# Performance work log

Measured on AMD Instinct MI355X. Metric: run time of the kernel, lower is better.

Reference implementation:

```python
import jax, jax.numpy as jnp
import numpy as np

TAU = 1.0
EPS = 1e-8  # F.cosine_similarity eps


def _cl(X, Y):
    # Pairwise cosine similarity via L2-normalize + single GEMM (N,D)@(D,N)
    Xn = X / jnp.maximum(jnp.linalg.norm(X, axis=1, keepdims=True), EPS)
    Yn = Y / jnp.maximum(jnp.linalg.norm(Y, axis=1, keepdims=True), EPS)
    sim = Xn @ Yn.T  # [N, N], sim[i, j] = cos(X_i, Y_j)
    e = jnp.exp(sim / TAU)
    pos = jnp.diagonal(e)               # exp(diag(sim)/tau), [N]
    neg = jnp.sum(e, axis=0) - pos      # column sums minus positive, [N]
    return -jnp.log(pos / neg).reshape(X.shape[0], 1)


def setup_inputs() -> dict:
    key = jax.random.key(0)
    ks = jax.random.split(key, 6)
    N, D1, D2, DO = 8192, 1024, 768, 256
    X = jax.random.normal(ks[0], (N, D1), dtype=jnp.float32)
    Y = jax.random.normal(ks[1], (N, D2), dtype=jnp.float32)
    # nn.Linear params (kaiming-uniform-ish scale)
    Wx = jax.random.uniform(ks[2], (DO, D1), jnp.float32, -1, 1) / np.sqrt(D1)
    bx = jax.random.uniform(ks[3], (DO,), jnp.float32, -1, 1) / np.sqrt(D1)
    Wy = jax.random.uniform(ks[4], (DO, D2), jnp.float32, -1, 1) / np.sqrt(D2)
    by = jax.random.uniform(ks[5], (DO,), jnp.float32, -1, 1) / np.sqrt(D2)
    return {"X": X, "Y": Y, "Wx": Wx, "bx": bx, "Wy": Wy, "by": by}


def reference(X, Y, Wx, bx, Wy, by):
    Xp = X @ Wx.T + bx  # proj_x
    Yp = Y @ Wy.T + by  # proj_y
    return _cl(Xp, Yp) + _cl(Yp, Xp)  # [N, 1]
```

## Files before the change

### kernel.cpp

```cpp
#include <hip/hip_runtime.h>
#include <hip/hip_bf16.h>

typedef __bf16 bf16_t;
typedef __bf16 bf16x8 __attribute__((ext_vector_type(8)));
typedef float  f32x4  __attribute__((ext_vector_type(4)));
typedef unsigned long u64;
typedef u64 u64x2 __attribute__((ext_vector_type(2)));

__device__ __forceinline__ bf16x8 pack8(f32x4 a, f32x4 b) {
    bf16x8 h = { (bf16_t)a.x, (bf16_t)a.y, (bf16_t)a.z, (bf16_t)a.w,
                 (bf16_t)b.x, (bf16_t)b.y, (bf16_t)b.z, (bf16_t)b.w };
    return h;
}

__device__ __forceinline__ void gl_lds16(const void* g, void* l) {
    __builtin_amdgcn_global_load_lds(
        (const __attribute__((address_space(1))) unsigned int*)g,
        (__attribute__((address_space(3))) unsigned int*)l, 16, 0, 0);
}

#if __has_builtin(__builtin_amdgcn_cvt_pk_fp8_f32)
__device__ __forceinline__ unsigned char cvt1_e4m3(float x) {
    return (unsigned char)(__builtin_amdgcn_cvt_pk_fp8_f32(x, x, 0, false) & 0xff);
}
#else
__device__ __forceinline__ unsigned char cvt1_e4m3(float x) {
    unsigned u = __float_as_uint(x);
    unsigned sign = (u >> 24) & 0x80u;
    float a = fabsf(x);
    if (a < 7.8125e-3f) { int q = (int)(a * 512.0f + 0.5f); return (unsigned char)(sign | q); }
    if (a >= 448.0f) return (unsigned char)(sign | 0x7E);
    unsigned au = u & 0x7FFFFFFFu;
    unsigned lsb = (au >> 20) & 1u;
    au += 0x7FFFFu + lsb;
    int exp = (int)(au >> 23) - 127;
    unsigned man = (au >> 20) & 7u;
    return (unsigned char)(sign | ((unsigned)(exp + 7) << 3) | man);
}
#endif

__device__ __forceinline__ int frag_off_k(int row16, int k) {
    return ((k >> 6) << 10) + (((k >> 3) & 3) << 8) + (row16 << 4)
         + (((k >> 5) & 1) << 3) + (k & 7);
}

__global__ __launch_bounds__(256) void wconv(
    const float* __restrict__ Wx, const float* __restrict__ Wy,
    bf16_t* __restrict__ Wxt, bf16_t* __restrict__ Wyt,
    float* __restrict__ sums)
{
    int id = blockIdx.x * 256 + threadIdx.x;
    if (blockIdx.x < 64) sums[id] = 0.0f;

    int row, k0, K;
    const float* W;
    bf16_t* Wt;
    if (id < 32768) { W = Wx; Wt = Wxt; K = 1024; row = id >> 7; k0 = (id & 127) << 3; }
    else { int c = id - 32768; W = Wy; Wt = Wyt; K = 768; row = c / 96; k0 = (c % 96) << 3; }

    f32x4 lo = *reinterpret_cast<const f32x4*>(&W[(size_t)row * K + k0]);
    f32x4 hi = *reinterpret_cast<const f32x4*>(&W[(size_t)row * K + k0 + 4]);
    size_t off = (size_t)(row >> 4) * 16 * K + frag_off_k(row & 15, k0);
    *reinterpret_cast<bf16x8*>(Wt + off) = pack8(lo, hi);
}

__global__ __launch_bounds__(512, 4) void proj_norm(
    const float* __restrict__ X, const float* __restrict__ Y,
    const bf16_t* __restrict__ Wxt, const float* __restrict__ bxp,
    const bf16_t* __restrict__ Wyt, const float* __restrict__ byp,
    unsigned char* __restrict__ Xt, unsigned char* __restrict__ Yt)
{
    __shared__ float Abuf[2][32 * 64];
    __shared__ unsigned char obuf[8192];
    __shared__ float ssqL[4][32];

    const int tid  = threadIdx.x;
    const int lane = tid & 63;
    const int wave = tid >> 6;
    const int quad = lane >> 4;
    const int c16  = lane & 15;
    const int rg   = wave >> 2;
    const int cg   = wave & 3;

    const bool isY = blockIdx.x >= 256;
    const float*  A    = isY ? Y   : X;
    const bf16_t* Wt   = isY ? Wyt : Wxt;
    const float*  bias = isY ? byp : bxp;
    unsigned char* dst = isY ? Yt  : Xt;
    const int K = isY ? 768 : 1024;
    const int S = K >> 6;
    const int rowBase = (blockIdx.x & 255) * 32;

    auto stage = [&](int s, int b) {
        int r0  = wave * 4;
        int row = r0 + (lane >> 4);
        int gch = (lane & 15) ^ (row & 15);
        gl_lds16(&A[(size_t)(rowBase + row) * K + s * 64 + gch * 4],
                 &Abuf[b][r0 * 64]);
    };

    auto aFrag = [&](int b, int s2) -> bf16x8 {
        int row = rg * 16 + c16;
        int e   = s2 * 8 + quad * 2;
        const float* base = &Abuf[b][row * 64];
        f32x4 lo = *reinterpret_cast<const f32x4*>(base + ((e ^ c16) << 2));
        f32x4 hi = *reinterpret_cast<const f32x4*>(base + (((e + 1) ^ c16) << 2));
        return pack8(lo, hi);
    };

    const bf16_t* pB[4];
    #pragma unroll
    for (int nf = 0; nf < 4; ++nf)
        pB[nf] = Wt + (size_t)(cg * 4 + nf) * 16 * K + quad * 256 + c16 * 16;

    f32x4 acc[4] = {};
    stage(0, 0);

    for (int s = 0; s < S; ++s) {
        const int b = s & 1;
        __syncthreads();
        if (s + 1 < S) stage(s + 1, b ^ 1);
        #pragma unroll
        for (int s2 = 0; s2 < 2; ++s2) {
            bf16x8 aF = aFrag(b, s2);
            #pragma unroll
            for (int nf = 0; nf < 4; ++nf) {
                bf16x8 bF = *reinterpret_cast<const bf16x8*>(pB[nf] + s * 1024 + s2 * 8);
                acc[nf] = __builtin_amdgcn_mfma_f32_16x16x32_bf16(aF, bF, acc[nf], 0, 0, 0);
            }
        }
    }

    #pragma unroll
    for (int nf = 0; nf < 4; ++nf) {
        float bb = bias[cg * 64 + nf * 16 + c16];
        #pragma unroll
        for (int r = 0; r < 4; ++r) acc[nf][r] += bb;
    }

    #pragma unroll
    for (int r = 0; r < 4; ++r) {
        float v = 0.f;
        #pragma unroll
        for (int nf = 0; nf < 4; ++nf) v += acc[nf][r] * acc[nf][r];
        v += __shfl_xor(v, 1, 64);
        v += __shfl_xor(v, 2, 64);
        v += __shfl_xor(v, 4, 64);
        v += __shfl_xor(v, 8, 64);
        if (c16 == 0) ssqL[cg][rg * 16 + quad * 4 + r] = v;
    }
    __syncthreads();

    #pragma unroll
    for (int r = 0; r < 4; ++r) {
        int lr = rg * 16 + quad * 4 + r;
        float t = ssqL[0][lr] + ssqL[1][lr] + ssqL[2][lr] + ssqL[3][lr];
        float inv = 1.0f / fmaxf(sqrtf(t), 1e-8f);
        #pragma unroll
        for (int nf = 0; nf < 4; ++nf) {
            int k = cg * 64 + nf * 16 + c16;
            obuf[((lr >> 4) << 12) + frag_off_k(lr & 15, k)] =
                cvt1_e4m3(acc[nf][r] * inv);
        }
    }
    __syncthreads();

    const f32x4* src = reinterpret_cast<const f32x4*>(&obuf[tid * 16]);
    f32x4* g = reinterpret_cast<f32x4*>(dst + (size_t)rowBase * 256 + tid * 16);
    g[0] = src[0];
}

__global__ __launch_bounds__(256) void sim_gemm(
    const unsigned char* __restrict__ Xt, const unsigned char* __restrict__ Yt,
    float* __restrict__ rowsum, float* __restrict__ colsum,
    float* __restrict__ pos)
{
    __shared__ float red[256];

    const int tid  = threadIdx.x;
    const int lane = tid & 63;
    const int wave = tid >> 6;
    const int quad = lane >> 4;
    const int c16  = lane & 15;
    const int wy   = wave >> 1;
    const int wx   = wave & 1;
    const int rowBase = blockIdx.x * 128;
    const int colBase = blockIdx.y * 128;

    const u64x2* pa[4];
    const u64x2* pb[4];
    #pragma unroll
    for (int mf = 0; mf < 4; ++mf)
        pa[mf] = reinterpret_cast<const u64x2*>(
            Xt + (size_t)(rowBase + wy * 64 + mf * 16) * 256 + quad * 256 + c16 * 16);
    #pragma unroll
    for (int nf = 0; nf < 4; ++nf)
        pb[nf] = reinterpret_cast<const u64x2*>(
            Yt + (size_t)(colBase + wx * 64 + nf * 16) * 256 + quad * 256 + c16 * 16);

    f32x4 acc[4][4] = {};

    auto loadf = [&](u64x2* A, u64x2* B, int slab) {
        #pragma unroll
        for (int i = 0; i < 4; ++i) {
            A[i] = pa[i][slab * 64];
            B[i] = pb[i][slab * 64];
        }
    };
    auto mm = [&](const u64x2* A, const u64x2* B) {
        #pragma unroll
        for (int mf = 0; mf < 4; ++mf)
            #pragma unroll
            for (int nf = 0; nf < 4; ++nf)
                acc[mf][nf] = __builtin_amdgcn_mfma_f32_16x16x32_fp8_fp8(
                    (long)A[mf].x, (long)B[nf].x, acc[mf][nf], 0, 0, 0);
        #pragma unroll
        for (int mf = 0; mf < 4; ++mf)
            #pragma unroll
            for (int nf = 0; nf < 4; ++nf)
                acc[mf][nf] = __builtin_amdgcn_mfma_f32_16x16x32_fp8_fp8(
                    (long)A[mf].y, (long)B[nf].y, acc[mf][nf], 0, 0, 0);
    };

    u64x2 A0[4], B0[4], A1[4], B1[4];
    loadf(A0, B0, 0);
    loadf(A1, B1, 1);
    mm(A0, B0);
    loadf(A0, B0, 2);
    mm(A1, B1);
    loadf(A1, B1, 3);
    mm(A0, B0);
    mm(A1, B1);

    #pragma unroll
    for (int mf = 0; mf < 4; ++mf)
        #pragma unroll
        for (int nf = 0; nf < 4; ++nf)
            #pragma unroll
            for (int r = 0; r < 4; ++r)
                acc[mf][nf][r] = __expf(acc[mf][nf][r]);

    if (rowBase == colBase) {
        #pragma unroll
        for (int mf = 0; mf < 4; ++mf)
            #pragma unroll
            for (int nf = 0; nf < 4; ++nf)
                #pragma unroll
                for (int r = 0; r < 4; ++r) {
                    int lrow = wy * 64 + mf * 16 + quad * 4 + r;
                    int lcol = wx * 64 + nf * 16 + c16;
                    if (lrow == lcol) pos[rowBase + lrow] = acc[mf][nf][r];
                }
    }

    float rs[4][4];
    #pragma unroll
    for (int mf = 0; mf < 4; ++mf)
        #pragma unroll
        for (int r = 0; r < 4; ++r) {
            float v = acc[mf][0][r] + acc[mf][1][r] + acc[mf][2][r] + acc[mf][3][r];
            v += __shfl_xor(v, 1, 64);
            v += __shfl_xor(v, 2, 64);
            v += __shfl_xor(v, 4, 64);
            v += __shfl_xor(v, 8, 64);
            rs[mf][r] = v;
        }

    float cs[4];
    #pragma unroll
    for (int nf = 0; nf < 4; ++nf) {
        float v = 0.f;
        #pragma unroll
        for (int mf = 0; mf < 4; ++mf)
            #pragma unroll
            for (int r = 0; r < 4; ++r)
                v += acc[mf][nf][r];
        v += __shfl_xor(v, 16, 64);
        v += __shfl_xor(v, 32, 64);
        cs[nf] = v;
    }

    red[tid] = 0.f;
    __syncthreads();

    if (c16 == 0) {
        #pragma unroll
        for (int mf = 0; mf < 4; ++mf)
            #pragma unroll
            for (int r = 0; r < 4; ++r)
                atomicAdd(&red[wy * 64 + mf * 16 + quad * 4 + r], rs[mf][r]);
    }
    if (quad == 0) {
        #pragma unroll
        for (int nf = 0; nf < 4; ++nf)
            atomicAdd(&red[128 + wx * 64 + nf * 16 + c16], cs[nf]);
    }
    __syncthreads();

    if (tid < 128) atomicAdd(&rowsum[rowBase + tid], red[tid]);
    else           atomicAdd(&colsum[colBase + tid - 128], red[tid]);
}

__global__ __launch_bounds__(256) void finalize(
    const float* __restrict__ rowsum, const float* __restrict__ colsum,
    const float* __restrict__ pos, float* __restrict__ out)
{
    int i = blockIdx.x * 256 + threadIdx.x;
    float p = pos[i];
    out[i] = logf(colsum[i] - p) + logf(rowsum[i] - p) - 2.0f * logf(p);
}

extern "C" void kernel_launch(void* const* d_in, const int* in_sizes, int n_in,
                              void* d_out, int out_size, void* d_ws, size_t ws_size,
                              hipStream_t stream) {
    const float* X  = (const float*)d_in[0];
    const float* Y  = (const float*)d_in[1];
    const float* Wx = (const float*)d_in[2];
    const float* bx = (const float*)d_in[3];
    const float* Wy = (const float*)d_in[4];
    const float* by = (const float*)d_in[5];
    float* out = (float*)d_out;

    char* ws = (char*)d_ws;
    unsigned char* Xt  = (unsigned char*)(ws);
    unsigned char* Yt  = (unsigned char*)(ws + (2u << 20));
    bf16_t*        Wxt = (bf16_t*)(ws + (4u << 20));
    bf16_t*        Wyt = (bf16_t*)(ws + (4u << 20) + (512u << 10));
    float* rowsum = (float*)(ws + (5u << 20));
    float* colsum = rowsum + 8192;
    float* pos    = colsum + 8192;

    wconv<<<224, 256, 0, stream>>>(Wx, Wy, Wxt, Wyt, rowsum);
    proj_norm<<<512, 512, 0, stream>>>(X, Y, Wxt, bx, Wyt, by, Xt, Yt);
    sim_gemm<<<dim3(64, 64), 256, 0, stream>>>(Xt, Yt, rowsum, colsum, pos);
    finalize<<<32, 256, 0, stream>>>(rowsum, colsum, pos, out);
}
```

Before: 172.1 us.

## Load projection A operands directly to registers with register double-buffering

The projection kernel drops the LDS staging of X/Y tiles via global_load_lds and __syncthreads, and instead has each lane load its A fragment straight from global memory into registers. A and B fragments are double-buffered in registers across K-steps. Blocks shrink to 256 threads covering 16 rows, with twice as many blocks launched. This removes per-step barriers and LDS traffic, but the fp32 A rows are now read with strided per-lane accesses and register pressure goes up.

```diff
diff --git a/kernel.cpp b/kernel.cpp
--- a/kernel.cpp
+++ b/kernel.cpp
@@ -11,12 +11,6 @@
     bf16x8 h = { (bf16_t)a.x, (bf16_t)a.y, (bf16_t)a.z, (bf16_t)a.w,
                  (bf16_t)b.x, (bf16_t)b.y, (bf16_t)b.z, (bf16_t)b.w };
     return h;
-}
-
-__device__ __forceinline__ void gl_lds16(const void* g, void* l) {
-    __builtin_amdgcn_global_load_lds(
-        (const __attribute__((address_space(1))) unsigned int*)g,
-        (__attribute__((address_space(3))) unsigned int*)l, 16, 0, 0);
 }
 
 #if __has_builtin(__builtin_amdgcn_cvt_pk_fp8_f32)
@@ -64,71 +58,73 @@
     *reinterpret_cast<bf16x8*>(Wt + off) = pack8(lo, hi);
 }
 
-__global__ __launch_bounds__(512, 4) void proj_norm(
+__global__ __launch_bounds__(256) void proj_norm(
     const float* __restrict__ X, const float* __restrict__ Y,
     const bf16_t* __restrict__ Wxt, const float* __restrict__ bxp,
     const bf16_t* __restrict__ Wyt, const float* __restrict__ byp,
     unsigned char* __restrict__ Xt, unsigned char* __restrict__ Yt)
 {
-    __shared__ float Abuf[2][32 * 64];
-    __shared__ unsigned char obuf[8192];
-    __shared__ float ssqL[4][32];
+    __shared__ unsigned char obuf[4096];
+    __shared__ float ssqL[4][16];
 
     const int tid  = threadIdx.x;
     const int lane = tid & 63;
-    const int wave = tid >> 6;
+    const int cg   = tid >> 6;
     const int quad = lane >> 4;
     const int c16  = lane & 15;
-    const int rg   = wave >> 2;
-    const int cg   = wave & 3;
-
-    const bool isY = blockIdx.x >= 256;
+
+    const bool isY = blockIdx.x >= 512;
     const float*  A    = isY ? Y   : X;
     const bf16_t* Wt   = isY ? Wyt : Wxt;
     const float*  bias = isY ? byp : bxp;
     unsigned char* dst = isY ? Yt  : Xt;
     const int K = isY ? 768 : 1024;
     const int S = K >> 6;
-    const int rowBase = (blockIdx.x & 255) * 32;
-
-    auto stage = [&](int s, int b) {
-        int r0  = wave * 4;
-        int row = r0 + (lane >> 4);
-        int gch = (lane & 15) ^ (row & 15);
-        gl_lds16(&A[(size_t)(rowBase + row) * K + s * 64 + gch * 4],
-                 &Abuf[b][r0 * 64]);
-    };
-
-    auto aFrag = [&](int b, int s2) -> bf16x8 {
-        int row = rg * 16 + c16;
-        int e   = s2 * 8 + quad * 2;
-        const float* base = &Abuf[b][row * 64];
-        f32x4 lo = *reinterpret_cast<const f32x4*>(base + ((e ^ c16) << 2));
-        f32x4 hi = *reinterpret_cast<const f32x4*>(base + (((e + 1) ^ c16) << 2));
-        return pack8(lo, hi);
-    };
-
+    const int rowBase = (blockIdx.x & 511) * 16;
+
+    const float* pA = A + (size_t)(rowBase + c16) * K + quad * 8;
     const bf16_t* pB[4];
     #pragma unroll
     for (int nf = 0; nf < 4; ++nf)
         pB[nf] = Wt + (size_t)(cg * 4 + nf) * 16 * K + quad * 256 + c16 * 16;
 
-    f32x4 acc[4] = {};
-    stage(0, 0);
-
-    for (int s = 0; s < S; ++s) {
-        const int b = s & 1;
-        __syncthreads();
-        if (s + 1 < S) stage(s + 1, b ^ 1);
-        #pragma unroll
-        for (int s2 = 0; s2 < 2; ++s2) {
-            bf16x8 aF = aFrag(b, s2);
-            #pragma unroll
-            for (int nf = 0; nf < 4; ++nf) {
-                bf16x8 bF = *reinterpret_cast<const bf16x8*>(pB[nf] + s * 1024 + s2 * 8);
-                acc[nf] = __builtin_amdgcn_mfma_f32_16x16x32_bf16(aF, bF, acc[nf], 0, 0, 0);
-            }
+    f32x4  a0[4], a1[4];
+    bf16x8 b0[4][2], b1[4][2];
+    f32x4  acc[4] = {};
+
+    auto loadA = [&](f32x4* av, int s) {
+        const float* q = pA + s * 64;
+        av[0] = *reinterpret_cast<const f32x4*>(q);
+        av[1] = *reinterpret_cast<const f32x4*>(q + 4);
+        av[2] = *reinterpret_cast<const f32x4*>(q + 32);
+        av[3] = *reinterpret_cast<const f32x4*>(q + 36);
+    };
+    auto loadB = [&](bf16x8 (*bv)[2], int s) {
+        #pragma unroll
+        for (int nf = 0; nf < 4; ++nf) {
+            const bf16_t* p = pB[nf] + s * 1024;
+            bv[nf][0] = *reinterpret_cast<const bf16x8*>(p);
+            bv[nf][1] = *reinterpret_cast<const bf16x8*>(p + 8);
         }
+    };
+    auto step = [&](const f32x4* av, const bf16x8 (*bv)[2]) {
+        bf16x8 aF0 = pack8(av[0], av[1]);
+        #pragma unroll
+        for (int nf = 0; nf < 4; ++nf)
+            acc[nf] = __builtin_amdgcn_mfma_f32_16x16x32_bf16(aF0, bv[nf][0], acc[nf], 0, 0, 0);
+        bf16x8 aF1 = pack8(av[2], av[3]);
+        #pragma unroll
+        for (int nf = 0; nf < 4; ++nf)
+            acc[nf] = __builtin_amdgcn_mfma_f32_16x16x32_bf16(aF1, bv[nf][1], acc[nf], 0, 0, 0);
+    };
+
+    loadA(a0, 0);
+    loadB(b0, 0);
+    for (int s = 0; s < S; s += 2) {
+        if (s + 1 < S) { loadA(a1, s + 1); loadB(b1, s + 1); }
+        step(a0, b0);
+        if (s + 2 < S) { loadA(a0, s + 2); loadB(b0, s + 2); }
+        step(a1, b1);
     }
 
     #pragma unroll
@@ -147,27 +143,25 @@
         v += __shfl_xor(v, 2, 64);
         v += __shfl_xor(v, 4, 64);
         v += __shfl_xor(v, 8, 64);
-        if (c16 == 0) ssqL[cg][rg * 16 + quad * 4 + r] = v;
+        if (c16 == 0) ssqL[cg][quad * 4 + r] = v;
     }
     __syncthreads();
 
     #pragma unroll
     for (int r = 0; r < 4; ++r) {
-        int lr = rg * 16 + quad * 4 + r;
-        float t = ssqL[0][lr] + ssqL[1][lr] + ssqL[2][lr] + ssqL[3][lr];
+        int row16 = quad * 4 + r;
+        float t = ssqL[0][row16] + ssqL[1][row16] + ssqL[2][row16] + ssqL[3][row16];
         float inv = 1.0f / fmaxf(sqrtf(t), 1e-8f);
         #pragma unroll
         for (int nf = 0; nf < 4; ++nf) {
             int k = cg * 64 + nf * 16 + c16;
-            obuf[((lr >> 4) << 12) + frag_off_k(lr & 15, k)] =
-                cvt1_e4m3(acc[nf][r] * inv);
+            obuf[frag_off_k(row16, k)] = cvt1_e4m3(acc[nf][r] * inv);
         }
     }
     __syncthreads();
 
-    const f32x4* src = reinterpret_cast<const f32x4*>(&obuf[tid * 16]);
-    f32x4* g = reinterpret_cast<f32x4*>(dst + (size_t)rowBase * 256 + tid * 16);
-    g[0] = src[0];
+    *reinterpret_cast<f32x4*>(dst + (size_t)rowBase * 256 + tid * 16) =
+        *reinterpret_cast<const f32x4*>(&obuf[tid * 16]);
 }
 
 __global__ __launch_bounds__(256) void sim_gemm(
@@ -331,7 +325,7 @@
     float* pos    = colsum + 8192;
 
     wconv<<<224, 256, 0, stream>>>(Wx, Wy, Wxt, Wyt, rowsum);
-    proj_norm<<<512, 512, 0, stream>>>(X, Y, Wxt, bx, Wyt, by, Xt, Yt);
+    proj_norm<<<1024, 256, 0, stream>>>(X, Y, Wxt, bx, Wyt, by, Xt, Yt);
     sim_gemm<<<dim3(64, 64), 256, 0, stream>>>(Xt, Yt, rowsum, colsum, pos);
     finalize<<<32, 256, 0, stream>>>(rowsum, colsum, pos, out);
 }
```

After: 176.3 us. 2.5% more time.
